# Performance work log

Hardware: AMD Instinct MI355X
Metric: run time of the kernel (lower is better)

Reference implementation:

```python
import jax, jax.numpy as jnp
import numpy as np

M_TOKENS, D_IN, D_OUT = 4096, 4096, 16384


def setup_inputs() -> dict:
    key = jax.random.key(0)
    k1, k2, k3, k4 = jax.random.split(key, 4)
    x = jax.random.normal(k1, (M_TOKENS, D_IN), dtype=jnp.float32)
    # pre-quantized int8 weight, stored [K, N] as in qweight_kn
    qweight_kn = jax.random.randint(k2, (D_IN, D_OUT), -127, 128, dtype=jnp.int8)
    # per-output-channel weight dequant scales (float16 buffer, used as fp32 in kernel)
    weight_scales = jax.random.uniform(k3, (D_OUT,), dtype=jnp.float32, minval=1e-3, maxval=2e-2)
    bias = jax.random.normal(k4, (D_OUT,), dtype=jnp.float32) * 0.01
    return {"x": x, "qweight_kn": qweight_kn, "weight_scales": weight_scales, "bias": bias}


def reference(x, qweight_kn, weight_scales, bias):
    target_dtype = x.dtype
    x2 = x.reshape(-1, x.shape[-1])  # [M, K]
    # dynamic per-token (per-row) symmetric quantization
    x_max = jnp.max(jnp.abs(x2), axis=-1, keepdims=True).astype(jnp.float32) + 1e-5
    x_scales = x_max / 127.0  # [M, 1]
    x_int8 = jnp.clip(jnp.round(x2.astype(jnp.float32) / x_scales), -128, 127).astype(jnp.int8)
    acc = jax.lax.dot_general(
        x_int8, qweight_kn,
        dimension_numbers=(((1,), (0,)), ((), ())),
        preferred_element_type=jnp.int32,
    )  # [M, N] int32
    # fused dequant: row act-scale * col weight-scale, plus bias
    c = acc.astype(jnp.float32) * x_scales * weight_scales[None, :].astype(jnp.float32)
    c = c + bias[None, :]
    out = c.astype(jnp.bfloat16)  # kernel stores bf16
    return out.reshape(*x.shape[:-1], -1).astype(target_dtype)
```

## Files before the change

kernel.cpp:

```cpp
#include <hip/hip_runtime.h>
#include <hip/hip_bf16.h>
#include <stdint.h>

typedef int v4i __attribute__((ext_vector_type(4)));

#define GM 4096
#define GN 16384
#define GK 4096
#define BM 256
#define BN 256
#define BK 64
#define NT (GK / BK)
#define SLOT_BYTES 16384

__device__ __forceinline__ void gload16(const void* g, void* l) {
  __builtin_amdgcn_global_load_lds(
      (const __attribute__((address_space(1))) void*)g,
      (__attribute__((address_space(3))) void*)l, 16, 0, 0);
}

__global__ __launch_bounds__(256) void quant_rows(
    const float* __restrict__ x, int8_t* __restrict__ xq,
    float* __restrict__ xs, int K) {
  const int row = blockIdx.x;
  const int t = threadIdx.x;
  const float4* src = (const float4*)(x + (size_t)row * K) + t * 4;
  float4 v[4];
  float m = 0.f;
#pragma unroll
  for (int i = 0; i < 4; ++i) {
    v[i] = src[i];
    m = fmaxf(m, fmaxf(fmaxf(fabsf(v[i].x), fabsf(v[i].y)),
                       fmaxf(fabsf(v[i].z), fabsf(v[i].w))));
  }
#pragma unroll
  for (int off = 1; off < 64; off <<= 1)
    m = fmaxf(m, __shfl_xor(m, off, 64));
  __shared__ float wmax[4];
  if ((t & 63) == 0) wmax[t >> 6] = m;
  __syncthreads();
  const float gm = fmaxf(fmaxf(wmax[0], wmax[1]), fmaxf(wmax[2], wmax[3]));
  const float scale = (gm + 1e-5f) / 127.0f;
  if (t == 0) xs[row] = scale;
  unsigned packed[4];
#pragma unroll
  for (int i = 0; i < 4; ++i) {
    float fv[4] = {v[i].x, v[i].y, v[i].z, v[i].w};
    unsigned p = 0;
#pragma unroll
    for (int j = 0; j < 4; ++j) {
      int q = (int)rintf(fv[j] / scale);
      q = max(-128, min(127, q));
      p |= (unsigned)(q & 0xff) << (8 * j);
    }
    packed[i] = p;
  }
  *(int4*)(xq + (size_t)row * K + t * 16) =
      make_int4((int)packed[0], (int)packed[1], (int)packed[2], (int)packed[3]);
}

__global__ __launch_bounds__(256) void transpose_pack(
    const int* __restrict__ W32, int8_t* __restrict__ Wt, int K, int N) {
  __shared__ __align__(16) int8_t tile[64][80];
  const int t = threadIdx.x;
  const int n0 = blockIdx.x * 64;
  const int k0 = blockIdx.y * 64;
  const int ln = t & 63;
  const int wv = t >> 6;
#pragma unroll
  for (int it = 0; it < 16; ++it) {
    const int kk = wv * 16 + it;
    tile[ln][kk] = (int8_t)W32[(size_t)(k0 + kk) * N + n0 + ln];
  }
  __syncthreads();
  const int kb = wv * 16;
  const int4 v = *(const int4*)&tile[ln][kb];
  *(int4*)(Wt + (size_t)(n0 + ln) * K + k0 + kb) = v;
}

__global__ __launch_bounds__(512, 2) void gemm_i8(
    const int8_t* __restrict__ Xq, const int8_t* __restrict__ Wt,
    const float* __restrict__ xs, const float* __restrict__ wsc,
    const float* __restrict__ bias, float* __restrict__ C) {
  __shared__ __align__(16) int8_t lA[4][BM * BK];
  __shared__ __align__(16) int8_t lB[4][BN * BK];

  const int t = threadIdx.x;
  const int lane = t & 63;
  const int w = t >> 6;
  const int wr = w >> 2;
  const int wc = w & 3;
  const int fr = lane & 15;
  const int kg = lane >> 4;

  const int bid = blockIdx.x;
  const int xcd = bid & 7;
  const int q = bid >> 3;
  const int tm = q & 15;
  const int tn = xcd * 8 + (q >> 4);
  const size_t rowA0 = (size_t)tm * BM;
  const size_t rowB0 = (size_t)tn * BN;

  const int8_t* XqB = Xq + rowA0 * GK;
  const int8_t* WtB = Wt + rowB0 * GK;
  int srcOff[2], dstOff[2];
#pragma unroll
  for (int i = 0; i < 2; ++i) {
    const int slot0 = (w * 2 + i) * 64;
    const int slot = slot0 + lane;
    const int r = slot >> 2;
    const int c = (slot & 3) ^ (r & 3);
    srcOff[i] = r * GK + c * 16;
    dstOff[i] = slot0 * 16;
  }

#define STAGE(KT, SLOT)                                                     \
  {                                                                         \
    const int ko = (KT)*BK;                                                 \
    _Pragma("unroll") for (int i = 0; i < 2; ++i)                           \
        gload16(XqB + srcOff[i] + ko, &lA[(SLOT)][0] + dstOff[i]);          \
    _Pragma("unroll") for (int i = 0; i < 2; ++i)                           \
        gload16(WtB + srcOff[i] + ko, &lB[(SLOT)][0] + dstOff[i]);          \
  }

  const int ckk = (kg ^ (fr & 3)) * 16;

  v4i acc[8][4] = {};
  v4i areg[8], breg[4];

#define RD_A(MI, SLOT)                                                      \
  areg[MI] = *(const v4i*)&lA[(SLOT)][(wr * 128 + (MI)*16 + fr) * BK + ckk];
#define RD_B(NJ, SLOT)                                                      \
  breg[NJ] = *(const v4i*)&lB[(SLOT)][(wc * 64 + (NJ)*16 + fr) * BK + ckk];

#define SB __builtin_amdgcn_sched_barrier(0)

#define BODY(T, SLOT)                                                        \
  {                                                                         \
     \
    asm volatile("s_waitcnt vmcnt(8)" ::: "memory");                        \
    __builtin_amdgcn_s_barrier();                                           \
    STAGE(((T) + 3) & (NT - 1), ((SLOT) + 3) & 3);                          \
    SB;                                                                     \
    RD_A(0, SLOT); RD_A(1, SLOT); RD_A(2, SLOT); RD_A(3, SLOT);             \
    RD_B(0, SLOT); RD_B(1, SLOT);                                           \
    SB;                                                                     \
    RD_B(2, SLOT); RD_B(3, SLOT);                                           \
    SB;                                                                     \
    RD_A(4, SLOT); RD_A(5, SLOT); RD_A(6, SLOT); RD_A(7, SLOT);             \
    SB;                                                                     \
    asm volatile("s_waitcnt lgkmcnt(6)" ::: "memory");      \
    SB;                                                                     \
    __builtin_amdgcn_s_setprio(1);                                          \
    _Pragma("unroll") for (int mi = 0; mi < 4; ++mi)                        \
        _Pragma("unroll") for (int nj = 0; nj < 2; ++nj)                    \
            acc[mi][nj] = __builtin_amdgcn_mfma_i32_16x16x64_i8(            \
                areg[mi], breg[nj], acc[mi][nj], 0, 0, 0);                  \
    __builtin_amdgcn_s_setprio(0);                                          \
    asm volatile("s_waitcnt lgkmcnt(4)" ::: "memory");          \
    SB;                                                                     \
    __builtin_amdgcn_s_setprio(1);                                          \
    _Pragma("unroll") for (int mi = 0; mi < 4; ++mi)                        \
        _Pragma("unroll") for (int nj = 2; nj < 4; ++nj)                    \
            acc[mi][nj] = __builtin_amdgcn_mfma_i32_16x16x64_i8(            \
                areg[mi], breg[nj], acc[mi][nj], 0, 0, 0);                  \
    __builtin_amdgcn_s_setprio(0);                                          \
    asm volatile("s_waitcnt lgkmcnt(0)" ::: "memory");           \
    SB;                                                                     \
    __builtin_amdgcn_s_setprio(1);                                          \
    _Pragma("unroll") for (int mi = 4; mi < 8; ++mi)                        \
        _Pragma("unroll") for (int nj = 0; nj < 4; ++nj)                    \
            acc[mi][nj] = __builtin_amdgcn_mfma_i32_16x16x64_i8(            \
                areg[mi], breg[nj], acc[mi][nj], 0, 0, 0);                  \
    __builtin_amdgcn_s_setprio(0);                                          \
  }

  STAGE(0, 0);
  STAGE(1, 1);
  STAGE(2, 2);

  for (int kt = 0; kt < NT; kt += 4) {
    BODY(kt, 0);
    BODY(kt + 1, 1);
    BODY(kt + 2, 2);
    BODY(kt + 3, 3);
  }

#pragma unroll
  for (int nj = 0; nj < 4; ++nj) {
    const int col_l = wc * 64 + nj * 16 + fr;
    const float wsv = wsc[rowB0 + col_l];
    const float bv = bias[rowB0 + col_l];
#pragma unroll
    for (int mi = 0; mi < 8; ++mi) {
#pragma unroll
      for (int r = 0; r < 4; ++r) {
        const size_t row = rowA0 + wr * 128 + mi * 16 + kg * 4 + r;
        const float f = (float)acc[mi][nj][r] * xs[row] * wsv + bv;
        C[row * GN + rowB0 + col_l] = __bfloat162float(__float2bfloat16(f));
      }
    }
  }
}

extern "C" void kernel_launch(void* const* d_in, const int* in_sizes, int n_in,
                              void* d_out, int out_size, void* d_ws, size_t ws_size,
                              hipStream_t stream) {
  const int M = GM, K = GK, N = GN;
  const float* x = (const float*)d_in[0];
  const int* W32 = (const int*)d_in[1];
  const float* wsc = (const float*)d_in[2];
  const float* bias = (const float*)d_in[3];
  float* out = (float*)d_out;

  float* xs = (float*)d_ws;
  int8_t* Xq = (int8_t*)d_ws + 16384;
  int8_t* Wt = (int8_t*)d_ws + 16384 + (size_t)M * K;

  transpose_pack<<<dim3(N / 64, K / 64), 256, 0, stream>>>(W32, Wt, K, N);
  quant_rows<<<M, 256, 0, stream>>>(x, Xq, xs, K);
  gemm_i8<<<dim3((M / BM) * (N / BN)), 512, 0, stream>>>(Xq, Wt, xs, wsc, bias,
                                                         out);
}
```

Before: 503.4 us.

## Prepack B in MFMA fragment order and load it directly into registers

```diff
diff --git a/kernel.cpp b/kernel.cpp
--- a/kernel.cpp
+++ b/kernel.cpp
@@ -11,7 +11,6 @@
 #define BN 256
 #define BK 64
 #define NT (GK / BK)
-#define SLOT_BYTES 16384
 
 __device__ __forceinline__ void gload16(const void* g, void* l) {
   __builtin_amdgcn_global_load_lds(
@@ -60,7 +59,7 @@
 }
 
 __global__ __launch_bounds__(256) void transpose_pack(
-    const int* __restrict__ W32, int8_t* __restrict__ Wt, int K, int N) {
+    const int* __restrict__ W32, int8_t* __restrict__ Wt2, int K, int N) {
   __shared__ __align__(16) int8_t tile[64][80];
   const int t = threadIdx.x;
   const int n0 = blockIdx.x * 64;
@@ -73,17 +72,19 @@
     tile[ln][kk] = (int8_t)W32[(size_t)(k0 + kk) * N + n0 + ln];
   }
   __syncthreads();
-  const int kb = wv * 16;
-  const int4 v = *(const int4*)&tile[ln][kb];
-  *(int4*)(Wt + (size_t)(n0 + ln) * K + k0 + kb) = v;
+  const int lane = ln;
+  const int4 v = *(const int4*)&tile[wv * 16 + (lane & 15)][(lane >> 4) * 16];
+  const int tn = n0 >> 8;
+  const int kt = k0 >> 6;
+  const int f = ((n0 >> 4) & 15) + wv;
+  *(int4*)(Wt2 + (((size_t)(tn * 64 + kt) * 16 + f) * 64 + lane) * 16) = v;
 }
 
 __global__ __launch_bounds__(512, 2) void gemm_i8(
-    const int8_t* __restrict__ Xq, const int8_t* __restrict__ Wt,
+    const int8_t* __restrict__ Xq, const int8_t* __restrict__ Wt2,
     const float* __restrict__ xs, const float* __restrict__ wsc,
     const float* __restrict__ bias, float* __restrict__ C) {
   __shared__ __align__(16) int8_t lA[4][BM * BK];
-  __shared__ __align__(16) int8_t lB[4][BN * BK];
 
   const int t = threadIdx.x;
   const int lane = t & 63;
@@ -102,82 +103,82 @@
   const size_t rowB0 = (size_t)tn * BN;
 
   const int8_t* XqB = Xq + rowA0 * GK;
-  const int8_t* WtB = Wt + rowB0 * GK;
   int srcOff[2], dstOff[2];
 #pragma unroll
   for (int i = 0; i < 2; ++i) {
     const int slot0 = (w * 2 + i) * 64;
     const int slot = slot0 + lane;
     const int r = slot >> 2;
-    const int c = (slot & 3) ^ (r & 3);
+    const int c = (slot & 3) ^ ((r >> 2) & 3);
     srcOff[i] = r * GK + c * 16;
     dstOff[i] = slot0 * 16;
   }
 
-#define STAGE(KT, SLOT)                                                     \
-  {                                                                         \
-    const int ko = (KT)*BK;                                                 \
-    _Pragma("unroll") for (int i = 0; i < 2; ++i)                           \
-        gload16(XqB + srcOff[i] + ko, &lA[(SLOT)][0] + dstOff[i]);          \
-    _Pragma("unroll") for (int i = 0; i < 2; ++i)                           \
-        gload16(WtB + srcOff[i] + ko, &lB[(SLOT)][0] + dstOff[i]);          \
-  }
-
-  const int ckk = (kg ^ (fr & 3)) * 16;
+#define STAGE(KT, SLOT)                                              \
+  {                                                                  \
+    const int ko = (KT)*BK;                                          \
+    _Pragma("unroll") for (int i = 0; i < 2; ++i)                    \
+        gload16(XqB + srcOff[i] + ko, &lA[(SLOT)][0] + dstOff[i]);   \
+  }
+
+  const int8_t* bq = Wt2 + (size_t)tn * 1048576 + wc * 4096 + lane * 16;
 
   v4i acc[8][4] = {};
-  v4i areg[8], breg[4];
-
-#define RD_A(MI, SLOT)                                                      \
+  v4i areg[8], breg[4][4];
+
+#define LOADB(KT, S)                                                          \
+  {                                                                           \
+    const int8_t* bp = bq + (size_t)(KT)*16384;                               \
+    _Pragma("unroll") for (int nj = 0; nj < 4; ++nj)                          \
+        asm volatile("global_load_dwordx4 %0, %1, off"                        \
+                     : "=v"(breg[S][nj])                                      \
+                     : "v"(bp + nj * 1024)                                    \
+                     : "memory");                                             \
+  }
+
+  const int ckk = (kg ^ (fr >> 2)) * 16;
+#define RD_A(MI, SLOT)                                                        \
   areg[MI] = *(const v4i*)&lA[(SLOT)][(wr * 128 + (MI)*16 + fr) * BK + ckk];
-#define RD_B(NJ, SLOT)                                                      \
-  breg[NJ] = *(const v4i*)&lB[(SLOT)][(wc * 64 + (NJ)*16 + fr) * BK + ckk];
 
 #define SB __builtin_amdgcn_sched_barrier(0)
 
-#define BODY(T, SLOT)                                                        \
-  {                                                                         \
-     \
-    asm volatile("s_waitcnt vmcnt(8)" ::: "memory");                        \
-    __builtin_amdgcn_s_barrier();                                           \
-    STAGE(((T) + 3) & (NT - 1), ((SLOT) + 3) & 3);                          \
-    SB;                                                                     \
-    RD_A(0, SLOT); RD_A(1, SLOT); RD_A(2, SLOT); RD_A(3, SLOT);             \
-    RD_B(0, SLOT); RD_B(1, SLOT);                                           \
-    SB;                                                                     \
-    RD_B(2, SLOT); RD_B(3, SLOT);                                           \
-    SB;                                                                     \
-    RD_A(4, SLOT); RD_A(5, SLOT); RD_A(6, SLOT); RD_A(7, SLOT);             \
-    SB;                                                                     \
-    asm volatile("s_waitcnt lgkmcnt(6)" ::: "memory");      \
-    SB;                                                                     \
-    __builtin_amdgcn_s_setprio(1);                                          \
-    _Pragma("unroll") for (int mi = 0; mi < 4; ++mi)                        \
-        _Pragma("unroll") for (int nj = 0; nj < 2; ++nj)                    \
-            acc[mi][nj] = __builtin_amdgcn_mfma_i32_16x16x64_i8(            \
-                areg[mi], breg[nj], acc[mi][nj], 0, 0, 0);                  \
-    __builtin_amdgcn_s_setprio(0);                                          \
-    asm volatile("s_waitcnt lgkmcnt(4)" ::: "memory");          \
-    SB;                                                                     \
-    __builtin_amdgcn_s_setprio(1);                                          \
-    _Pragma("unroll") for (int mi = 0; mi < 4; ++mi)                        \
-        _Pragma("unroll") for (int nj = 2; nj < 4; ++nj)                    \
-            acc[mi][nj] = __builtin_amdgcn_mfma_i32_16x16x64_i8(            \
-                areg[mi], breg[nj], acc[mi][nj], 0, 0, 0);                  \
-    __builtin_amdgcn_s_setprio(0);                                          \
-    asm volatile("s_waitcnt lgkmcnt(0)" ::: "memory");           \
-    SB;                                                                     \
-    __builtin_amdgcn_s_setprio(1);                                          \
-    _Pragma("unroll") for (int mi = 4; mi < 8; ++mi)                        \
-        _Pragma("unroll") for (int nj = 0; nj < 4; ++nj)                    \
-            acc[mi][nj] = __builtin_amdgcn_mfma_i32_16x16x64_i8(            \
-                areg[mi], breg[nj], acc[mi][nj], 0, 0, 0);                  \
-    __builtin_amdgcn_s_setprio(0);                                          \
+#define BODY(T, SLOT)                                                         \
+  {                                                                           \
+         \
+    asm volatile("s_waitcnt vmcnt(12)" ::: "memory");                         \
+    __builtin_amdgcn_s_barrier();       \
+    SB;                                                                       \
+    STAGE(((T) + 3) & (NT - 1), ((SLOT) + 3) & 3);                            \
+    LOADB(((T) + 3) & (NT - 1), ((SLOT) + 3) & 3);                            \
+    SB;                                                                       \
+    RD_A(0, SLOT); RD_A(1, SLOT); RD_A(2, SLOT); RD_A(3, SLOT);               \
+    SB;                                                                       \
+    RD_A(4, SLOT); RD_A(5, SLOT); RD_A(6, SLOT); RD_A(7, SLOT);               \
+    SB;                                                                       \
+    asm volatile("s_waitcnt lgkmcnt(4)" ::: "memory");        \
+    SB;                                                                       \
+    __builtin_amdgcn_s_setprio(1);                                            \
+    _Pragma("unroll") for (int mi = 0; mi < 4; ++mi)                          \
+        _Pragma("unroll") for (int nj = 0; nj < 4; ++nj)                      \
+            acc[mi][nj] = __builtin_amdgcn_mfma_i32_16x16x64_i8(              \
+                areg[mi], breg[SLOT][nj], acc[mi][nj], 0, 0, 0);              \
+    __builtin_amdgcn_s_setprio(0);                                            \
+    asm volatile("s_waitcnt lgkmcnt(0)" ::: "memory");        \
+    SB;                                                                       \
+    __builtin_amdgcn_s_setprio(1);                                            \
+    _Pragma("unroll") for (int mi = 4; mi < 8; ++mi)                          \
+        _Pragma("unroll") for (int nj = 0; nj < 4; ++nj)                      \
+            acc[mi][nj] = __builtin_amdgcn_mfma_i32_16x16x64_i8(              \
+                areg[mi], breg[SLOT][nj], acc[mi][nj], 0, 0, 0);              \
+    __builtin_amdgcn_s_setprio(0);                                            \
   }
 
   STAGE(0, 0);
+  LOADB(0, 0);
   STAGE(1, 1);
+  LOADB(1, 1);
   STAGE(2, 2);
+  LOADB(2, 2);
 
   for (int kt = 0; kt < NT; kt += 4) {
     BODY(kt, 0);
@@ -185,6 +186,8 @@
     BODY(kt + 2, 2);
     BODY(kt + 3, 3);
   }
+  asm volatile("s_waitcnt vmcnt(0) lgkmcnt(0)" ::: "memory");
+  SB;
 
 #pragma unroll
   for (int nj = 0; nj < 4; ++nj) {
@@ -215,10 +218,10 @@
 
   float* xs = (float*)d_ws;
   int8_t* Xq = (int8_t*)d_ws + 16384;
-  int8_t* Wt = (int8_t*)d_ws + 16384 + (size_t)M * K;
-
-  transpose_pack<<<dim3(N / 64, K / 64), 256, 0, stream>>>(W32, Wt, K, N);
+  int8_t* Wt2 = (int8_t*)d_ws + 16384 + (size_t)M * K;
+
+  transpose_pack<<<dim3(N / 64, K / 64), 256, 0, stream>>>(W32, Wt2, K, N);
   quant_rows<<<M, 256, 0, stream>>>(x, Xq, xs, K);
-  gemm_i8<<<dim3((M / BM) * (N / BN)), 512, 0, stream>>>(Xq, Wt, xs, wsc, bias,
+  gemm_i8<<<dim3((M / BM) * (N / BN)), 512, 0, stream>>>(Xq, Wt2, xs, wsc, bias,
                                                          out);
 }
```

Result: faster. 433.2 us (-13.9%).
